# Kernel optimization log

Measured on AMD Instinct MI355X. Metric: run time of the kernel, lower is better.

Reference implementation:

```python
import jax, jax.numpy as jnp
import numpy as np

B, Q, K = 16, 64, 1024
QS = KS = VS = 256
H = 128
NEG = -1e6


def setup_inputs() -> dict:
    key = jax.random.key(0)
    ks = jax.random.split(key, 7)
    queries = jax.random.normal(ks[0], (B, Q, QS), dtype=jnp.float32)
    keys = jax.random.normal(ks[1], (B, K, KS), dtype=jnp.float32)
    values = jax.random.normal(ks[2], (B, K, VS), dtype=jnp.float32)
    valid_len = jax.random.randint(ks[3], (B,), 0, 512, dtype=jnp.int64)
    # Linear weights (PyTorch Linear stores (out, in); we store (in, out) for x @ W)
    Wq = jax.random.normal(ks[4], (QS, H), dtype=jnp.float32) / np.sqrt(QS)
    Wk = jax.random.normal(ks[5], (KS, H), dtype=jnp.float32) / np.sqrt(KS)
    Ws = jax.random.normal(ks[6], (H,), dtype=jnp.float32) / np.sqrt(H)
    return {"queries": queries, "keys": keys, "values": values,
            "valid_len": valid_len, "Wq": Wq, "Wk": Wk, "Ws": Ws}


def reference(queries, keys, values, valid_len, Wq, Wk, Ws):
    q = jnp.einsum('bqe,eh->bqh', queries, Wq)          # (B,Q,H)
    k = jnp.einsum('bke,eh->bkh', keys, Wk)             # (B,K,H)
    features = jnp.tanh(q[:, :, None, :] + k[:, None, :, :])  # (B,Q,K,H)
    scores = jnp.einsum('bqkh,h->bqk', features, Ws)    # (B,Q,K)
    # front_mask=True: mask the FIRST valid_len[b] key positions
    pos = jnp.arange(K)
    valid = pos[None, None, :] >= valid_len[:, None, None]  # (B,1,K)
    scores = jnp.where(valid, scores, NEG)
    attn = jax.nn.softmax(scores, axis=-1)              # (B,Q,K)
    return jnp.einsum('bqk,bkv->bqv', attn, values)     # (B,Q,VS)
```

## Files before the change

### kernel.cpp

```cpp
#include <hip/hip_runtime.h>

#define NB 16
#define NQ 64
#define NK 1024
#define ES 256
#define NH 128
#define VS 256
#define NEGV (-1e6f)

__device__ __forceinline__ float exp2_fast(float x) {
    float r; asm("v_exp_f32 %0, %1" : "=v"(r) : "v"(x)); return r;
}
__device__ __forceinline__ float rcp_fast(float x) {
    float r; asm("v_rcp_f32 %0, %1" : "=v"(r) : "v"(x)); return r;
}
__device__ __forceinline__ float tanh_fast(float x) {
    float e = exp2_fast(x * 2.885390081777927f);
    return fmaf(-2.0f, rcp_fast(1.0f + e), 1.0f);
}

__device__ __forceinline__ void fma4(float4& acc, const float4& wv, float s) {
    acc.x = fmaf(wv.x, s, acc.x);
    acc.y = fmaf(wv.y, s, acc.y);
    acc.z = fmaf(wv.z, s, acc.z);
    acc.w = fmaf(wv.w, s, acc.w);
}

__global__ __launch_bounds__(256) void proj_kernel(
    const float* __restrict__ queries, const float* __restrict__ keys,
    const float* __restrict__ Wq, const float* __restrict__ Wk,
    float* __restrict__ qp, float* __restrict__ kp)
{
    __shared__ __align__(16) float x_lds[16 * 256];
    const int bi  = blockIdx.x;
    const int tid = threadIdx.x;

    const float* src; const float* W; float* dst;
    if (bi < 64) {
        src = queries + (size_t)bi * 16 * ES;
        W   = Wq;
        dst = qp + (size_t)bi * 16 * NH;
    } else {
        const int r0 = (bi - 64) * 16;
        src = keys + (size_t)r0 * ES;
        W   = Wk;
        dst = kp + (size_t)r0 * NH;
    }

    const float4* s4 = (const float4*)src;
    float4* x4 = (float4*)x_lds;
#pragma unroll
    for (int i = 0; i < 4; ++i) x4[tid + i * 256] = s4[tid + i * 256];
    __syncthreads();

    const int h4 = tid & 31;
    const int g  = tid >> 5;
    const float* xa = x_lds + g * 256;
    const float* xb = x_lds + (g + 8) * 256;

    float4 a0 = {0, 0, 0, 0}, a1 = {0, 0, 0, 0};
    for (int e = 0; e < 256; e += 4) {
        const float4 va = *(const float4*)(xa + e);
        const float4 vb = *(const float4*)(xb + e);
#pragma unroll
        for (int j = 0; j < 4; ++j) {
            const float4 w4 = *(const float4*)(W + (size_t)(e + j) * NH + h4 * 4);
            const float fa = (j == 0) ? va.x : (j == 1) ? va.y : (j == 2) ? va.z : va.w;
            const float fb = (j == 0) ? vb.x : (j == 1) ? vb.y : (j == 2) ? vb.z : vb.w;
            fma4(a0, w4, fa);
            fma4(a1, w4, fb);
        }
    }
    *(float4*)(dst + (size_t)g * NH + h4 * 4)       = a0;
    *(float4*)(dst + (size_t)(g + 8) * NH + h4 * 4) = a1;
}

__global__ __launch_bounds__(256) void scores_kernel(
    const float* __restrict__ qp, const float* __restrict__ kp,
    const float* __restrict__ Ws, const int* __restrict__ valid_len,
    float* __restrict__ scores)
{
    __shared__ __align__(16) float kp_s[64 * 128];
    __shared__ __align__(16) float qp_s[8 * 128];
    __shared__ __align__(16) float ws_s[128];

    const int kt  = blockIdx.x;
    const int qt  = blockIdx.y;
    const int b   = blockIdx.z;
    const int tid = threadIdx.x;

    const float4* ksrc = (const float4*)(kp + (size_t)(b * NK + kt * 64) * NH);
#pragma unroll
    for (int i = 0; i < 8; ++i) {
        const int idx = tid + i * 256;
        const int row = idx >> 5, c = idx & 31;
        const float4 v = ksrc[idx];
        *(float4*)(kp_s + row * 128 + 4 * (c ^ (row & 7))) = v;
    }
    ((float4*)qp_s)[tid & 255] = ((const float4*)(qp + (size_t)(b * NQ + qt * 8) * NH))[tid & 255];
    if (tid < 32) ((float4*)ws_s)[tid] = ((const float4*)Ws)[tid];
    __syncthreads();

    const int lane = tid & 63;
    const int w    = tid >> 6;
    const float* qa = qp_s + w * 128;
    const float* qb = qp_s + (w + 4) * 128;
    const float* kr = kp_s + lane * 128;
    const int sw = lane & 7;

    float s0 = 0.f, s1 = 0.f;
#pragma unroll
    for (int c = 0; c < 32; ++c) {
        const float4 kv = *(const float4*)(kr + 4 * (c ^ sw));
        const float4 va = *(const float4*)(qa + 4 * c);
        const float4 vb = *(const float4*)(qb + 4 * c);
        const float4 wv = *(const float4*)(ws_s + 4 * c);
        s0 = fmaf(wv.x, tanh_fast(va.x + kv.x), s0);
        s0 = fmaf(wv.y, tanh_fast(va.y + kv.y), s0);
        s0 = fmaf(wv.z, tanh_fast(va.z + kv.z), s0);
        s0 = fmaf(wv.w, tanh_fast(va.w + kv.w), s0);
        s1 = fmaf(wv.x, tanh_fast(vb.x + kv.x), s1);
        s1 = fmaf(wv.y, tanh_fast(vb.y + kv.y), s1);
        s1 = fmaf(wv.z, tanh_fast(vb.z + kv.z), s1);
        s1 = fmaf(wv.w, tanh_fast(vb.w + kv.w), s1);
    }

    const int vl = valid_len[b];
    const int kg = kt * 64 + lane;
    const float o0 = (kg >= vl) ? s0 : NEGV;
    const float o1 = (kg >= vl) ? s1 : NEGV;
    scores[(size_t)(b * NQ + qt * 8 + w) * NK + kg]     = o0;
    scores[(size_t)(b * NQ + qt * 8 + w + 4) * NK + kg] = o1;
}

__global__ __launch_bounds__(256) void pv_kernel(
    const float* __restrict__ scores, const float* __restrict__ values,
    float* __restrict__ part, float* __restrict__ zpart)
{
    __shared__ __align__(16) float a_lds[8 * 256];
    const int ks  = blockIdx.x;
    const int qt  = blockIdx.y;
    const int b   = blockIdx.z;
    const int tid = threadIdx.x;

#pragma unroll
    for (int i = 0; i < 8; ++i) {
        const float s = scores[(size_t)(b * NQ + qt * 8 + i) * NK + ks * 256 + tid];
        a_lds[i * 256 + tid] = exp2_fast(s * 1.4426950408889634f);
    }
    __syncthreads();

    const int lane = tid & 63;
    const int w    = tid >> 6;
    float z0 = a_lds[w * 256 + lane] + a_lds[w * 256 + lane + 64] +
               a_lds[w * 256 + lane + 128] + a_lds[w * 256 + lane + 192];
    float z1 = a_lds[(w + 4) * 256 + lane] + a_lds[(w + 4) * 256 + lane + 64] +
               a_lds[(w + 4) * 256 + lane + 128] + a_lds[(w + 4) * 256 + lane + 192];
#pragma unroll
    for (int off = 32; off; off >>= 1) {
        z0 += __shfl_xor(z0, off);
        z1 += __shfl_xor(z1, off);
    }
    if (lane == 0) {
        zpart[(size_t)(b * NQ + qt * 8 + w) * 4 + ks]     = z0;
        zpart[(size_t)(b * NQ + qt * 8 + w + 4) * 4 + ks] = z1;
    }

    float acc[8] = {0, 0, 0, 0, 0, 0, 0, 0};
    const float* vbase = values + (size_t)(b * NK + ks * 256) * VS + tid;
#pragma unroll 2
    for (int kk = 0; kk < 256; kk += 4) {
        const float v0 = vbase[(size_t)(kk + 0) * VS];
        const float v1 = vbase[(size_t)(kk + 1) * VS];
        const float v2 = vbase[(size_t)(kk + 2) * VS];
        const float v3 = vbase[(size_t)(kk + 3) * VS];
#pragma unroll
        for (int i = 0; i < 8; ++i) {
            const float4 av = *(const float4*)(a_lds + i * 256 + kk);
            acc[i] = fmaf(av.x, v0, acc[i]);
            acc[i] = fmaf(av.y, v1, acc[i]);
            acc[i] = fmaf(av.z, v2, acc[i]);
            acc[i] = fmaf(av.w, v3, acc[i]);
        }
    }
#pragma unroll
    for (int i = 0; i < 8; ++i)
        part[((size_t)(b * NQ + qt * 8 + i) * 4 + ks) * VS + tid] = acc[i];
}

__global__ __launch_bounds__(256) void finish_kernel(
    const float* __restrict__ part, const float* __restrict__ zpart,
    float* __restrict__ out)
{
    const int r   = blockIdx.x;
    const int tid = threadIdx.x;
    const float z = zpart[r * 4 + 0] + zpart[r * 4 + 1] +
                    zpart[r * 4 + 2] + zpart[r * 4 + 3];
    const float s = part[(size_t)(r * 4 + 0) * VS + tid] +
                    part[(size_t)(r * 4 + 1) * VS + tid] +
                    part[(size_t)(r * 4 + 2) * VS + tid] +
                    part[(size_t)(r * 4 + 3) * VS + tid];
    out[(size_t)r * VS + tid] = s / z;
}

extern "C" void kernel_launch(void* const* d_in, const int* in_sizes, int n_in,
                              void* d_out, int out_size, void* d_ws, size_t ws_size,
                              hipStream_t stream)
{
    (void)in_sizes; (void)n_in; (void)out_size; (void)ws_size;
    const float* queries = (const float*)d_in[0];
    const float* keys    = (const float*)d_in[1];
    const float* values  = (const float*)d_in[2];
    const int*   vlen    = (const int*)d_in[3];
    const float* Wq      = (const float*)d_in[4];
    const float* Wk      = (const float*)d_in[5];
    const float* Ws      = (const float*)d_in[6];
    float* out = (float*)d_out;

    float* qp     = (float*)d_ws;
    float* kp     = qp + 131072;
    float* scores = kp + 2097152;
    float* zpart  = scores + 1048576;
    float* part   = zpart + 4096;

    proj_kernel<<<1088, 256, 0, stream>>>(queries, keys, Wq, Wk, qp, kp);
    scores_kernel<<<dim3(16, 8, 16), 256, 0, stream>>>(qp, kp, Ws, vlen, scores);
    pv_kernel<<<dim3(4, 8, 16), 256, 0, stream>>>(scores, values, part, zpart);
    finish_kernel<<<1024, 256, 0, stream>>>(part, zpart, out);
}
```

Before: 171.2 us.

## Fold tanh into sigmoid form, fuse exp into scores, retile PV with transposed probabilities

Rewrites the additive-attention score using tanh = 1 - 2*sigmoid, folding scale constants into the projection outputs and the Ws vector so each element needs only exp, add and rcp. Exponentiation and masking move into the scores kernel, which writes unnormalized probabilities transposed by key. The PV kernel is retiled to 32 queries by 128 keys with more accumulators per thread, and the projection kernel processes 32 rows per block. The exp is taken without subtracting a max, relying on scores being bounded, and the part buffer aliases the kp workspace.

```diff
diff --git a/kernel.cpp b/kernel.cpp
--- a/kernel.cpp
+++ b/kernel.cpp
@@ -6,7 +6,8 @@
 #define ES 256
 #define NH 128
 #define VS 256
-#define NEGV (-1e6f)
+#define SCALE2 2.885390081777927f
+#define L2E    1.4426950408889634f
 
 __device__ __forceinline__ float exp2_fast(float x) {
     float r; asm("v_exp_f32 %0, %1" : "=v"(r) : "v"(x)); return r;
@@ -14,11 +15,6 @@
 __device__ __forceinline__ float rcp_fast(float x) {
     float r; asm("v_rcp_f32 %0, %1" : "=v"(r) : "v"(x)); return r;
 }
-__device__ __forceinline__ float tanh_fast(float x) {
-    float e = exp2_fast(x * 2.885390081777927f);
-    return fmaf(-2.0f, rcp_fast(1.0f + e), 1.0f);
-}
-
 __device__ __forceinline__ void fma4(float4& acc, const float4& wv, float s) {
     acc.x = fmaf(wv.x, s, acc.x);
     acc.y = fmaf(wv.y, s, acc.y);
@@ -31,17 +27,17 @@
     const float* __restrict__ Wq, const float* __restrict__ Wk,
     float* __restrict__ qp, float* __restrict__ kp)
 {
-    __shared__ __align__(16) float x_lds[16 * 256];
+    __shared__ __align__(16) float x_lds[32 * 256];
     const int bi  = blockIdx.x;
     const int tid = threadIdx.x;
 
     const float* src; const float* W; float* dst;
-    if (bi < 64) {
-        src = queries + (size_t)bi * 16 * ES;
+    if (bi < 32) {
+        src = queries + (size_t)bi * 32 * ES;
         W   = Wq;
-        dst = qp + (size_t)bi * 16 * NH;
+        dst = qp + (size_t)bi * 32 * NH;
     } else {
-        const int r0 = (bi - 64) * 16;
+        const int r0 = (bi - 32) * 32;
         src = keys + (size_t)r0 * ES;
         W   = Wk;
         dst = kp + (size_t)r0 * NH;
@@ -50,35 +46,50 @@
     const float4* s4 = (const float4*)src;
     float4* x4 = (float4*)x_lds;
 #pragma unroll
-    for (int i = 0; i < 4; ++i) x4[tid + i * 256] = s4[tid + i * 256];
+    for (int i = 0; i < 8; ++i) x4[tid + i * 256] = s4[tid + i * 256];
     __syncthreads();
 
     const int h4 = tid & 31;
     const int g  = tid >> 5;
-    const float* xa = x_lds + g * 256;
-    const float* xb = x_lds + (g + 8) * 256;
-
-    float4 a0 = {0, 0, 0, 0}, a1 = {0, 0, 0, 0};
+    const float* x0 = x_lds + (g +  0) * 256;
+    const float* x1 = x_lds + (g +  8) * 256;
+    const float* x2 = x_lds + (g + 16) * 256;
+    const float* x3 = x_lds + (g + 24) * 256;
+
+    float4 a0 = {0,0,0,0}, a1 = {0,0,0,0}, a2 = {0,0,0,0}, a3 = {0,0,0,0};
+#pragma unroll 4
     for (int e = 0; e < 256; e += 4) {
-        const float4 va = *(const float4*)(xa + e);
-        const float4 vb = *(const float4*)(xb + e);
+        const float4 v0 = *(const float4*)(x0 + e);
+        const float4 v1 = *(const float4*)(x1 + e);
+        const float4 v2 = *(const float4*)(x2 + e);
+        const float4 v3 = *(const float4*)(x3 + e);
 #pragma unroll
         for (int j = 0; j < 4; ++j) {
             const float4 w4 = *(const float4*)(W + (size_t)(e + j) * NH + h4 * 4);
-            const float fa = (j == 0) ? va.x : (j == 1) ? va.y : (j == 2) ? va.z : va.w;
-            const float fb = (j == 0) ? vb.x : (j == 1) ? vb.y : (j == 2) ? vb.z : vb.w;
-            fma4(a0, w4, fa);
-            fma4(a1, w4, fb);
+            const float f0 = (j==0)?v0.x:(j==1)?v0.y:(j==2)?v0.z:v0.w;
+            const float f1 = (j==0)?v1.x:(j==1)?v1.y:(j==2)?v1.z:v1.w;
+            const float f2 = (j==0)?v2.x:(j==1)?v2.y:(j==2)?v2.z:v2.w;
+            const float f3 = (j==0)?v3.x:(j==1)?v3.y:(j==2)?v3.z:v3.w;
+            fma4(a0, w4, f0); fma4(a1, w4, f1);
+            fma4(a2, w4, f2); fma4(a3, w4, f3);
         }
     }
-    *(float4*)(dst + (size_t)g * NH + h4 * 4)       = a0;
-    *(float4*)(dst + (size_t)(g + 8) * NH + h4 * 4) = a1;
+    const float c = SCALE2;
+    float4 o;
+    o.x=a0.x*c; o.y=a0.y*c; o.z=a0.z*c; o.w=a0.w*c;
+    *(float4*)(dst + (size_t)(g +  0) * NH + h4 * 4) = o;
+    o.x=a1.x*c; o.y=a1.y*c; o.z=a1.z*c; o.w=a1.w*c;
+    *(float4*)(dst + (size_t)(g +  8) * NH + h4 * 4) = o;
+    o.x=a2.x*c; o.y=a2.y*c; o.z=a2.z*c; o.w=a2.w*c;
+    *(float4*)(dst + (size_t)(g + 16) * NH + h4 * 4) = o;
+    o.x=a3.x*c; o.y=a3.y*c; o.z=a3.z*c; o.w=a3.w*c;
+    *(float4*)(dst + (size_t)(g + 24) * NH + h4 * 4) = o;
 }
 
 __global__ __launch_bounds__(256) void scores_kernel(
     const float* __restrict__ qp, const float* __restrict__ kp,
     const float* __restrict__ Ws, const int* __restrict__ valid_len,
-    float* __restrict__ scores)
+    float* __restrict__ pT)
 {
     __shared__ __align__(16) float kp_s[64 * 128];
     __shared__ __align__(16) float qp_s[8 * 128];
@@ -98,94 +109,110 @@
         *(float4*)(kp_s + row * 128 + 4 * (c ^ (row & 7))) = v;
     }
     ((float4*)qp_s)[tid & 255] = ((const float4*)(qp + (size_t)(b * NQ + qt * 8) * NH))[tid & 255];
-    if (tid < 32) ((float4*)ws_s)[tid] = ((const float4*)Ws)[tid];
+    if (tid < 32) {
+        float4 t = ((const float4*)Ws)[tid];
+        t.x *= -2.f; t.y *= -2.f; t.z *= -2.f; t.w *= -2.f;
+        ((float4*)ws_s)[tid] = t;
+    }
     __syncthreads();
 
     const int lane = tid & 63;
     const int w    = tid >> 6;
+
+    float sw = ws_s[lane] + ws_s[lane + 64];
+#pragma unroll
+    for (int off = 32; off; off >>= 1) sw += __shfl_xor(sw, off);
+    const float sW = -0.5f * sw;
+
     const float* qa = qp_s + w * 128;
     const float* qb = qp_s + (w + 4) * 128;
     const float* kr = kp_s + lane * 128;
-    const int sw = lane & 7;
+    const int sw_x = lane & 7;
 
     float s0 = 0.f, s1 = 0.f;
 #pragma unroll
     for (int c = 0; c < 32; ++c) {
-        const float4 kv = *(const float4*)(kr + 4 * (c ^ sw));
+        const float4 kv = *(const float4*)(kr + 4 * (c ^ sw_x));
         const float4 va = *(const float4*)(qa + 4 * c);
         const float4 vb = *(const float4*)(qb + 4 * c);
         const float4 wv = *(const float4*)(ws_s + 4 * c);
-        s0 = fmaf(wv.x, tanh_fast(va.x + kv.x), s0);
-        s0 = fmaf(wv.y, tanh_fast(va.y + kv.y), s0);
-        s0 = fmaf(wv.z, tanh_fast(va.z + kv.z), s0);
-        s0 = fmaf(wv.w, tanh_fast(va.w + kv.w), s0);
-        s1 = fmaf(wv.x, tanh_fast(vb.x + kv.x), s1);
-        s1 = fmaf(wv.y, tanh_fast(vb.y + kv.y), s1);
-        s1 = fmaf(wv.z, tanh_fast(vb.z + kv.z), s1);
-        s1 = fmaf(wv.w, tanh_fast(vb.w + kv.w), s1);
+        s0 = fmaf(wv.x, rcp_fast(1.0f + exp2_fast(va.x + kv.x)), s0);
+        s0 = fmaf(wv.y, rcp_fast(1.0f + exp2_fast(va.y + kv.y)), s0);
+        s0 = fmaf(wv.z, rcp_fast(1.0f + exp2_fast(va.z + kv.z)), s0);
+        s0 = fmaf(wv.w, rcp_fast(1.0f + exp2_fast(va.w + kv.w)), s0);
+        s1 = fmaf(wv.x, rcp_fast(1.0f + exp2_fast(vb.x + kv.x)), s1);
+        s1 = fmaf(wv.y, rcp_fast(1.0f + exp2_fast(vb.y + kv.y)), s1);
+        s1 = fmaf(wv.z, rcp_fast(1.0f + exp2_fast(vb.z + kv.z)), s1);
+        s1 = fmaf(wv.w, rcp_fast(1.0f + exp2_fast(vb.w + kv.w)), s1);
     }
 
     const int vl = valid_len[b];
     const int kg = kt * 64 + lane;
-    const float o0 = (kg >= vl) ? s0 : NEGV;
-    const float o1 = (kg >= vl) ? s1 : NEGV;
-    scores[(size_t)(b * NQ + qt * 8 + w) * NK + kg]     = o0;
-    scores[(size_t)(b * NQ + qt * 8 + w + 4) * NK + kg] = o1;
+    const float p0 = (kg >= vl) ? exp2_fast((sW + s0) * L2E) : 0.0f;
+    const float p1 = (kg >= vl) ? exp2_fast((sW + s1) * L2E) : 0.0f;
+    pT[((size_t)b * NK + kg) * NQ + qt * 8 + w]     = p0;
+    pT[((size_t)b * NK + kg) * NQ + qt * 8 + w + 4] = p1;
 }
 
 __global__ __launch_bounds__(256) void pv_kernel(
-    const float* __restrict__ scores, const float* __restrict__ values,
+    const float* __restrict__ pT, const float* __restrict__ values,
     float* __restrict__ part, float* __restrict__ zpart)
 {
-    __shared__ __align__(16) float a_lds[8 * 256];
-    const int ks  = blockIdx.x;
-    const int qt  = blockIdx.y;
+    __shared__ __align__(16) float a_s[128][36];
+    __shared__ float zp_s[4][32];
+    const int kt  = blockIdx.x;
+    const int qh  = blockIdx.y;
     const int b   = blockIdx.z;
     const int tid = threadIdx.x;
 
-#pragma unroll
-    for (int i = 0; i < 8; ++i) {
-        const float s = scores[(size_t)(b * NQ + qt * 8 + i) * NK + ks * 256 + tid];
-        a_lds[i * 256 + tid] = exp2_fast(s * 1.4426950408889634f);
-    }
-    __syncthreads();
-
-    const int lane = tid & 63;
-    const int w    = tid >> 6;
-    float z0 = a_lds[w * 256 + lane] + a_lds[w * 256 + lane + 64] +
-               a_lds[w * 256 + lane + 128] + a_lds[w * 256 + lane + 192];
-    float z1 = a_lds[(w + 4) * 256 + lane] + a_lds[(w + 4) * 256 + lane + 64] +
-               a_lds[(w + 4) * 256 + lane + 128] + a_lds[(w + 4) * 256 + lane + 192];
-#pragma unroll
-    for (int off = 32; off; off >>= 1) {
-        z0 += __shfl_xor(z0, off);
-        z1 += __shfl_xor(z1, off);
-    }
-    if (lane == 0) {
-        zpart[(size_t)(b * NQ + qt * 8 + w) * 4 + ks]     = z0;
-        zpart[(size_t)(b * NQ + qt * 8 + w + 4) * 4 + ks] = z1;
-    }
-
-    float acc[8] = {0, 0, 0, 0, 0, 0, 0, 0};
-    const float* vbase = values + (size_t)(b * NK + ks * 256) * VS + tid;
-#pragma unroll 2
-    for (int kk = 0; kk < 256; kk += 4) {
-        const float v0 = vbase[(size_t)(kk + 0) * VS];
-        const float v1 = vbase[(size_t)(kk + 1) * VS];
-        const float v2 = vbase[(size_t)(kk + 2) * VS];
-        const float v3 = vbase[(size_t)(kk + 3) * VS];
-#pragma unroll
-        for (int i = 0; i < 8; ++i) {
-            const float4 av = *(const float4*)(a_lds + i * 256 + kk);
-            acc[i] = fmaf(av.x, v0, acc[i]);
-            acc[i] = fmaf(av.y, v1, acc[i]);
-            acc[i] = fmaf(av.z, v2, acc[i]);
-            acc[i] = fmaf(av.w, v3, acc[i]);
+    {
+        const int q4 = (tid & 7) * 4;
+        const int k0 = tid >> 3;
+#pragma unroll
+        for (int i = 0; i < 4; ++i) {
+            const int k = k0 + 32 * i;
+            const float4 v = *(const float4*)(
+                pT + ((size_t)b * NK + kt * 128 + k) * NQ + qh * 32 + q4);
+            *(float4*)(&a_s[k][q4]) = v;
         }
     }
-#pragma unroll
-    for (int i = 0; i < 8; ++i)
-        part[((size_t)(b * NQ + qt * 8 + i) * 4 + ks) * VS + tid] = acc[i];
+    __syncthreads();
+
+    {
+        const int lane = tid & 63;
+        const int w    = tid >> 6;
+        const int qq   = lane & 31;
+        float z = 0.f;
+#pragma unroll
+        for (int i = 0; i < 32; ++i) z += a_s[w * 32 + i][qq];
+        if (lane < 32) zp_s[w][qq] = z;
+    }
+    __syncthreads();
+    if (tid < 32) {
+        const float zf = zp_s[0][tid] + zp_s[1][tid] + zp_s[2][tid] + zp_s[3][tid];
+        zpart[((size_t)kt * NB + b) * NQ + qh * 32 + tid] = zf;
+    }
+
+    float acc[32];
+#pragma unroll
+    for (int i = 0; i < 32; ++i) acc[i] = 0.f;
+
+    const float* vb = values + ((size_t)b * NK + kt * 128) * VS + tid;
+#pragma unroll 4
+    for (int k = 0; k < 128; ++k) {
+        const float v = vb[(size_t)k * VS];
+#pragma unroll
+        for (int j = 0; j < 8; ++j) {
+            const float4 a = *(const float4*)(&a_s[k][4 * j]);
+            acc[4*j+0] = fmaf(a.x, v, acc[4*j+0]);
+            acc[4*j+1] = fmaf(a.y, v, acc[4*j+1]);
+            acc[4*j+2] = fmaf(a.z, v, acc[4*j+2]);
+            acc[4*j+3] = fmaf(a.w, v, acc[4*j+3]);
+        }
+    }
+#pragma unroll
+    for (int q = 0; q < 32; ++q)
+        part[(((size_t)kt * NB + b) * NQ + qh * 32 + q) * VS + tid] = acc[q];
 }
 
 __global__ __launch_bounds__(256) void finish_kernel(
@@ -194,12 +221,13 @@
 {
     const int r   = blockIdx.x;
     const int tid = threadIdx.x;
-    const float z = zpart[r * 4 + 0] + zpart[r * 4 + 1] +
-                    zpart[r * 4 + 2] + zpart[r * 4 + 3];
-    const float s = part[(size_t)(r * 4 + 0) * VS + tid] +
-                    part[(size_t)(r * 4 + 1) * VS + tid] +
-                    part[(size_t)(r * 4 + 2) * VS + tid] +
-                    part[(size_t)(r * 4 + 3) * VS + tid];
+    const int b = r >> 6, q = r & 63;
+    float z = 0.f, s = 0.f;
+#pragma unroll
+    for (int kt = 0; kt < 8; ++kt) {
+        z += zpart[((size_t)kt * NB + b) * NQ + q];
+        s += part[(((size_t)kt * NB + b) * NQ + q) * VS + tid];
+    }
     out[(size_t)r * VS + tid] = s / z;
 }
 
@@ -217,14 +245,14 @@
     const float* Ws      = (const float*)d_in[6];
     float* out = (float*)d_out;
 
-    float* qp     = (float*)d_ws;
-    float* kp     = qp + 131072;
-    float* scores = kp + 2097152;
-    float* zpart  = scores + 1048576;
-    float* part   = zpart + 4096;
-
-    proj_kernel<<<1088, 256, 0, stream>>>(queries, keys, Wq, Wk, qp, kp);
-    scores_kernel<<<dim3(16, 8, 16), 256, 0, stream>>>(qp, kp, Ws, vlen, scores);
-    pv_kernel<<<dim3(4, 8, 16), 256, 0, stream>>>(scores, values, part, zpart);
+    float* qp    = (float*)d_ws;
+    float* kp    = qp + 131072;
+    float* part  = kp;
+    float* pT    = kp + 2097152;
+    float* zpart = pT + 1048576;
+
+    proj_kernel<<<544, 256, 0, stream>>>(queries, keys, Wq, Wk, qp, kp);
+    scores_kernel<<<dim3(16, 8, 16), 256, 0, stream>>>(qp, kp, Ws, vlen, pT);
+    pv_kernel<<<dim3(8, 2, 16), 256, 0, stream>>>(pT, values, part, zpart);
     finish_kernel<<<1024, 256, 0, stream>>>(part, zpart, out);
 }
```

Result: slower. 192.5 us (+12.4%).
